# Kernel tuning notes

Measured on AMD Instinct MI355X. Metric: run time of the kernel, lower is better.

The kernel has to match this reference:

```python
import jax, jax.numpy as jnp
import numpy as np

N_SERIES = 1024
N_TIME = 600
INPUT_SIZE = 168
OUTPUT_SIZE = 24
N_S = 4
SEAS = 24  # single seasonality period


def setup_inputs() -> dict:
    key = jax.random.key(0)
    k1, k2, k3 = jax.random.split(key, 3)
    # strictly positive series (Holt-Winters multiplicative form divides and logs)
    y = jax.random.uniform(k1, (N_SERIES, N_TIME), jnp.float32) + 0.5
    s_matrix = jax.random.normal(k2, (N_SERIES, N_S), jnp.float32)
    embeds = jax.random.uniform(k3, (N_SERIES, 1 + 1 + SEAS), jnp.float32)
    idxs = jnp.arange(N_SERIES, dtype=jnp.int32)
    return {"y": y, "s_matrix": s_matrix, "embeds": embeds, "idxs": idxs}


def _compute_levels_seasons(y, embeds_rows):
    # embeds_rows: (N, 26) = [lev_sms_logit, seas_sms_logit, 24 log init seasons]
    lev_sms = jax.nn.sigmoid(embeds_rows[:, 0])           # (N,)
    seas_sms = jax.nn.sigmoid(embeds_rows[:, 1])          # (N,)
    init_seas = jnp.exp(embeds_rows[:, 2:2 + SEAS])       # (N, P)

    level0 = y[:, 0] / init_seas[:, 0]                    # (N,)
    # buffer holds seasonalities1[t .. t+P-1]; before step t=1 that is
    # [init[1], ..., init[P-1], init[0]]
    buf0 = jnp.roll(init_seas, -1, axis=1)                # (N, P)

    def step(carry, y_t):
        lev_prev, buf = carry
        s_t = buf[:, 0]
        newlev = lev_sms * (y_t / s_t) + (1.0 - lev_sms) * lev_prev
        news = seas_sms * (y_t / newlev) + (1.0 - seas_sms) * s_t
        buf = jnp.concatenate([buf[:, 1:], news[:, None]], axis=1)
        return (newlev, buf), (newlev, news)

    (_, _), (levs, seas_new) = jax.lax.scan(step, (level0, buf0), y[:, 1:].T)
    levels = jnp.concatenate([level0[:, None], levs.T], axis=1)          # (N, T)
    # seasonalities1 indices 0..P are [init[0..P-1], init[0]], then one new per step
    seas_head = jnp.concatenate([init_seas, init_seas[:, :1]], axis=1)   # (N, P+1)
    seasonalities1 = jnp.concatenate([seas_head, seas_new.T], axis=1)    # (N, T+P)
    return levels, seasonalities1


def reference(y, s_matrix, embeds, idxs):
    embeds_rows = embeds[idxs]                                 # (N, 26)
    levels, seasonalities1 = _compute_levels_seasons(y, embeds_rows)

    n_series, n_time = y.shape
    n_windows = n_time - INPUT_SIZE - OUTPUT_SIZE + 1          # 409
    w = jnp.arange(n_windows)
    idx_in = w[:, None] + jnp.arange(INPUT_SIZE)               # (W, I)
    idx_out = w[:, None] + INPUT_SIZE + jnp.arange(OUTPUT_SIZE)  # (W, O)

    y_in = y[:, idx_in]                                        # (N, W, I)
    lev_end = levels[:, w + INPUT_SIZE - 1]                    # (N, W)
    seas_in = seasonalities1[:, idx_in]                        # (N, W, I)
    y_in_norm = jnp.log(y_in / (lev_end[:, :, None] * seas_in))
    insample = jnp.transpose(y_in_norm, (1, 0, 2))             # (W, N, I)
    static = jnp.broadcast_to(s_matrix[None], (n_windows, n_series, s_matrix.shape[1]))
    windows_y_insample = jnp.concatenate([insample, static], axis=2)  # (W, N, I+n_s)

    # eval mode: outsample windows are raw (un-normalized) targets
    windows_y_outsample = jnp.transpose(y[:, idx_out], (1, 0, 2))     # (W, N, O)

    return (windows_y_insample, windows_y_outsample, levels, seasonalities1)
```

## Files before the change

### kernel.cpp

```cpp
#include <hip/hip_runtime.h>

#define N_SERIES 1024
#define N_TIME 600
#define INPUT_SIZE 168
#define OUTPUT_SIZE 24
#define N_S 4
#define SEAS 24
#define N_WINDOWS (N_TIME - INPUT_SIZE - OUTPUT_SIZE + 1)
#define SEAS_LEN (N_TIME + SEAS)

#define INS_ELEMS (N_WINDOWS * N_SERIES * (INPUT_SIZE + N_S))
#define OUTS_ELEMS (N_WINDOWS * N_SERIES * OUTPUT_SIZE)
#define LEV_ELEMS (N_SERIES * N_TIME)
#define SEAS_ELEMS (N_SERIES * SEAS_LEN)

#define NQ_OUTS (OUTS_ELEMS / 4)
#define NQ_INS43 (N_WINDOWS * N_SERIES * 43)
#define INS_SLICE (NQ_INS43 / 8)

#define SCAN_BLOCKS 16
#define SCAN_T 64
#define COPY_BLOCKS 2032
#define INS_BLOCKS 2048
#define WS_NEEDED (2u * LEV_ELEMS * sizeof(float))

typedef float f4 __attribute__((ext_vector_type(4)));

#define WAVE_FENCE()                                   \
    do {                                               \
        __builtin_amdgcn_wave_barrier();               \
        asm volatile("" ::: "memory");                 \
    } while (0)

__global__ __launch_bounds__(SCAN_T) void scan_copy_kernel(
    const float* __restrict__ y, const float* __restrict__ embeds,
    const int* __restrict__ idxs, float* __restrict__ levels,
    float* __restrict__ seas1, f4* __restrict__ out_outs)
{
    __shared__ float b_lev[SCAN_T][25];
    __shared__ float b_sea[SCAN_T][25];

    if (blockIdx.x < SCAN_BLOCKS) {
        const int lane = threadIdx.x;
        const int s0 = blockIdx.x * SCAN_T;
        const int s = s0 + lane;
        const int row = idxs[s];
        const float* e = embeds + row * (2 + SEAS);

        const float lev_sms = 1.0f / (1.0f + __expf(-e[0]));
        const float seas_sms = 1.0f / (1.0f + __expf(-e[1]));
        const float one_m_lev = 1.0f - lev_sms;
        const float one_m_seas = 1.0f - seas_sms;

        const float* yrow = y + s * N_TIME;
        const f4* yv4 = (const f4*)yrow;

        f4 cur[6], nxt[6];
#pragma unroll
        for (int i = 0; i < 6; ++i) cur[i] = yv4[i];

        float sb[SEAS];
#pragma unroll
        for (int j = 0; j < SEAS; ++j) {
            float v = __expf(e[2 + j]);
            sb[j] = v;
            b_sea[lane][j] = v;
        }
        WAVE_FENCE();
#pragma unroll
        for (int k4 = 0; k4 < 6; ++k4) {
            int q4 = lane + k4 * SCAN_T;
            int r = q4 / 6;
            int c4 = q4 - r * 6;
            int cc = c4 * 4;
            f4 v = {b_sea[r][cc], b_sea[r][cc + 1], b_sea[r][cc + 2],
                    b_sea[r][cc + 3]};
            *(f4*)(seas1 + (s0 + r) * SEAS_LEN + cc) = v;
        }
        seas1[s * SEAS_LEN + SEAS] = sb[0];
        float lev = __fdividef(cur[0].x, sb[0]);
        levels[s * N_TIME] = lev;
        WAVE_FENCE();

        {
#pragma unroll
            for (int i = 0; i < 6; ++i) nxt[i] = yv4[6 + i];
#pragma unroll
            for (int j = 0; j < 23; ++j) {
                const int t = j + 1;
                float yt = cur[t >> 2][t & 3];
                float st = sb[t];
                float q1 = __fdividef(yt, st);
                float newlev = lev_sms * q1 + one_m_lev * lev;
                float news =
                    seas_sms * __fdividef(yt, newlev) + one_m_seas * st;
                lev = newlev;
                sb[t] = news;
                b_lev[lane][j] = newlev;
                b_sea[lane][j] = news;
            }
            WAVE_FENCE();
#pragma unroll
            for (int k = 0; k < 24; ++k) {
                int i = lane + k * SCAN_T;
                int r = i / 24;
                int col = i - r * 24;
                if (col < 23) {
                    int sr = s0 + r;
                    levels[sr * N_TIME + 1 + col] = b_lev[r][col];
                    seas1[sr * SEAS_LEN + 25 + col] = b_sea[r][col];
                }
            }
            WAVE_FENCE();
#pragma unroll
            for (int i = 0; i < 6; ++i) cur[i] = nxt[i];
        }

#pragma unroll 1
        for (int c = 1; c < 25; ++c) {
            const int t0 = 24 * c;
            if (c < 24) {
                const f4* p = (const f4*)(yrow + 24 * (c + 1));
#pragma unroll
                for (int i = 0; i < 6; ++i) nxt[i] = p[i];
            }
#pragma unroll
            for (int j = 0; j < 24; ++j) {
                float yt = cur[j >> 2][j & 3];
                float st = sb[j];
                float q1 = __fdividef(yt, st);
                float newlev = lev_sms * q1 + one_m_lev * lev;
                float news =
                    seas_sms * __fdividef(yt, newlev) + one_m_seas * st;
                lev = newlev;
                sb[j] = news;
                b_lev[lane][j] = newlev;
                b_sea[lane][j] = news;
            }
            WAVE_FENCE();
#pragma unroll
            for (int k4 = 0; k4 < 6; ++k4) {
                int q4 = lane + k4 * SCAN_T;
                int r = q4 / 6;
                int c4 = q4 - r * 6;
                int sr = s0 + r;
                int cc = c4 * 4;
                f4 vl = {b_lev[r][cc], b_lev[r][cc + 1], b_lev[r][cc + 2],
                         b_lev[r][cc + 3]};
                *(f4*)(levels + sr * N_TIME + t0 + cc) = vl;
                f4 vs = {b_sea[r][cc], b_sea[r][cc + 1], b_sea[r][cc + 2],
                         b_sea[r][cc + 3]};
                *(f4*)(seas1 + sr * SEAS_LEN + SEAS + t0 + cc) = vs;
            }
            WAVE_FENCE();
#pragma unroll
            for (int i = 0; i < 6; ++i) cur[i] = nxt[i];
        }
    } else {
        int idx = (blockIdx.x - SCAN_BLOCKS) * SCAN_T + threadIdx.x;
        const int stride = (gridDim.x - SCAN_BLOCKS) * SCAN_T;
        for (; idx < NQ_OUTS; idx += stride) {
            int rowq = idx / 6;
            int j4 = idx - rowq * 6;
            int w = rowq >> 10;
            int s = rowq & 1023;
            const float* yp = y + s * N_TIME + w + INPUT_SIZE + j4 * 4;
            f4 v = {yp[0], yp[1], yp[2], yp[3]};
            out_outs[idx] = v;
        }
    }
}

__global__ __launch_bounds__(256) void logpass_kernel(
    const float* __restrict__ y, const float* __restrict__ levels,
    const float* __restrict__ seas1, float* __restrict__ tbl,
    float* __restrict__ llv)
{
    int i = blockIdx.x * 256 + threadIdx.x;
    int sr = i / 150;
    int c = i - sr * 150;
    f4 a = *((const f4*)(y + sr * N_TIME) + c);
    f4 se = *((const f4*)(seas1 + sr * SEAS_LEN) + c);
    f4 l = *((const f4*)(levels + sr * N_TIME) + c);
    f4 ta, tl;
    ta.x = __logf(__fdividef(a.x, se.x));
    ta.y = __logf(__fdividef(a.y, se.y));
    ta.z = __logf(__fdividef(a.z, se.z));
    ta.w = __logf(__fdividef(a.w, se.w));
    tl.x = __logf(l.x);
    tl.y = __logf(l.y);
    tl.z = __logf(l.z);
    tl.w = __logf(l.w);
    ((f4*)tbl)[i] = ta;
    ((f4*)llv)[i] = tl;
}

__global__ __launch_bounds__(256) void ins_kernel(
    const float* __restrict__ tbl, const float* __restrict__ llv,
    const float* __restrict__ s_matrix, f4* __restrict__ out_ins)
{
    const f4* sm4 = (const f4*)s_matrix;
    const int xcd = blockIdx.x & 7;
    const int lb = blockIdx.x >> 3;
    const int qend = (xcd + 1) * INS_SLICE;
    const int stride = (INS_BLOCKS / 8) * 256;
    for (int q = xcd * INS_SLICE + lb * 256 + (int)threadIdx.x; q < qend;
         q += stride) {
        int rowq = q / 43;
        int e4 = q - rowq * 43;
        int w = rowq >> 10;
        int s = rowq & 1023;
        f4 v;
        if (e4 == 42) {
            v = sm4[s];
        } else {
            int t = w + e4 * 4;
            const float* tp = tbl + s * N_TIME + t;
            float lv = llv[s * N_TIME + w + INPUT_SIZE - 1];
            v.x = tp[0] - lv;
            v.y = tp[1] - lv;
            v.z = tp[2] - lv;
            v.w = tp[3] - lv;
        }
        out_ins[q] = v;
    }
}

__global__ __launch_bounds__(256) void ins_kernel_fb(
    const float* __restrict__ y, const float* __restrict__ levels,
    const float* __restrict__ seas1, const float* __restrict__ s_matrix,
    f4* __restrict__ out_ins)
{
    const f4* sm4 = (const f4*)s_matrix;
    const int xcd = blockIdx.x & 7;
    const int lb = blockIdx.x >> 3;
    const int qend = (xcd + 1) * INS_SLICE;
    const int stride = (INS_BLOCKS / 8) * 256;
    for (int q = xcd * INS_SLICE + lb * 256 + (int)threadIdx.x; q < qend;
         q += stride) {
        int rowq = q / 43;
        int e4 = q - rowq * 43;
        int w = rowq >> 10;
        int s = rowq & 1023;
        f4 v;
        if (e4 == 42) {
            v = sm4[s];
        } else {
            int t = w + e4 * 4;
            float lev = levels[s * N_TIME + w + INPUT_SIZE - 1];
            const float* yp = y + s * N_TIME + t;
            const float* sp = seas1 + s * SEAS_LEN + t;
            float vv[4];
#pragma unroll
            for (int j = 0; j < 4; ++j)
                vv[j] = __logf(__fdividef(yp[j], lev * sp[j]));
            v.x = vv[0]; v.y = vv[1]; v.z = vv[2]; v.w = vv[3];
        }
        out_ins[q] = v;
    }
}

extern "C" void kernel_launch(void* const* d_in, const int* in_sizes, int n_in,
                              void* d_out, int out_size, void* d_ws, size_t ws_size,
                              hipStream_t stream) {
    const float* y      = (const float*)d_in[0];
    const float* sm     = (const float*)d_in[1];
    const float* embeds = (const float*)d_in[2];
    const int*   idxs   = (const int*)d_in[3];

    float* out      = (float*)d_out;
    float* out_ins  = out;
    float* out_outs = out + INS_ELEMS;
    float* out_lev  = out + INS_ELEMS + OUTS_ELEMS;
    float* out_seas = out_lev + LEV_ELEMS;

    float* tbl = (float*)d_ws;
    float* llv = tbl + LEV_ELEMS;
    const int have_ws = (ws_size >= (size_t)WS_NEEDED) ? 1 : 0;

    scan_copy_kernel<<<SCAN_BLOCKS + COPY_BLOCKS, SCAN_T, 0, stream>>>(
        y, embeds, idxs, out_lev, out_seas, (f4*)out_outs);
    if (have_ws) {
        logpass_kernel<<<LEV_ELEMS / 4 / 256, 256, 0, stream>>>(
            y, out_lev, out_seas, tbl, llv);
        ins_kernel<<<INS_BLOCKS, 256, 0, stream>>>(tbl, llv, sm,
                                                   (f4*)out_ins);
    } else {
        ins_kernel_fb<<<INS_BLOCKS, 256, 0, stream>>>(y, out_lev, out_seas,
                                                      sm, (f4*)out_ins);
    }
}
```

Before: 111.3 us.

## Assign series pairs per block in insample kernel and use nontemporal stores

```diff
diff --git a/kernel.cpp b/kernel.cpp
--- a/kernel.cpp
+++ b/kernel.cpp
@@ -15,14 +15,16 @@
 #define SEAS_ELEMS (N_SERIES * SEAS_LEN)
 
 #define NQ_OUTS (OUTS_ELEMS / 4)
-#define NQ_INS43 (N_WINDOWS * N_SERIES * 43)
-#define INS_SLICE (NQ_INS43 / 8)
 
 #define SCAN_BLOCKS 16
 #define SCAN_T 64
 #define COPY_BLOCKS 2032
-#define INS_BLOCKS 2048
 #define WS_NEEDED (2u * LEV_ELEMS * sizeof(float))
+
+#define INS2_BLOCKS 512
+#define SGRP 2
+#define TASKS_PER_W (SGRP * 43)
+#define TASKS_PER_G (N_WINDOWS * TASKS_PER_W)
 
 typedef float f4 __attribute__((ext_vector_type(4)));
 
@@ -166,7 +168,7 @@
             int s = rowq & 1023;
             const float* yp = y + s * N_TIME + w + INPUT_SIZE + j4 * 4;
             f4 v = {yp[0], yp[1], yp[2], yp[3]};
-            out_outs[idx] = v;
+            __builtin_nontemporal_store(v, &out_outs[idx]);
         }
     }
 }
@@ -195,25 +197,23 @@
     ((f4*)llv)[i] = tl;
 }
 
-__global__ __launch_bounds__(256) void ins_kernel(
+__global__ __launch_bounds__(256) void ins2_kernel(
     const float* __restrict__ tbl, const float* __restrict__ llv,
-    const float* __restrict__ s_matrix, f4* __restrict__ out_ins)
+    const float* __restrict__ y, const float* __restrict__ levels,
+    const float* __restrict__ seas1, const float* __restrict__ s_matrix,
+    f4* __restrict__ out_ins, int have_ws)
 {
-    const f4* sm4 = (const f4*)s_matrix;
-    const int xcd = blockIdx.x & 7;
-    const int lb = blockIdx.x >> 3;
-    const int qend = (xcd + 1) * INS_SLICE;
-    const int stride = (INS_BLOCKS / 8) * 256;
-    for (int q = xcd * INS_SLICE + lb * 256 + (int)threadIdx.x; q < qend;
-         q += stride) {
-        int rowq = q / 43;
-        int e4 = q - rowq * 43;
-        int w = rowq >> 10;
-        int s = rowq & 1023;
+    const int s0 = blockIdx.x * SGRP;
+    for (int ql = threadIdx.x; ql < TASKS_PER_G; ql += 256) {
+        int w = ql / TASKS_PER_W;
+        int slot = ql - w * TASKS_PER_W;
+        int sl = slot / 43;
+        int e4 = slot - sl * 43;
+        int s = s0 + sl;
         f4 v;
         if (e4 == 42) {
-            v = sm4[s];
-        } else {
+            v = *(const f4*)(s_matrix + s * N_S);
+        } else if (have_ws) {
             int t = w + e4 * 4;
             const float* tp = tbl + s * N_TIME + t;
             float lv = llv[s * N_TIME + w + INPUT_SIZE - 1];
@@ -221,42 +221,17 @@
             v.y = tp[1] - lv;
             v.z = tp[2] - lv;
             v.w = tp[3] - lv;
-        }
-        out_ins[q] = v;
-    }
-}
-
-__global__ __launch_bounds__(256) void ins_kernel_fb(
-    const float* __restrict__ y, const float* __restrict__ levels,
-    const float* __restrict__ seas1, const float* __restrict__ s_matrix,
-    f4* __restrict__ out_ins)
-{
-    const f4* sm4 = (const f4*)s_matrix;
-    const int xcd = blockIdx.x & 7;
-    const int lb = blockIdx.x >> 3;
-    const int qend = (xcd + 1) * INS_SLICE;
-    const int stride = (INS_BLOCKS / 8) * 256;
-    for (int q = xcd * INS_SLICE + lb * 256 + (int)threadIdx.x; q < qend;
-         q += stride) {
-        int rowq = q / 43;
-        int e4 = q - rowq * 43;
-        int w = rowq >> 10;
-        int s = rowq & 1023;
-        f4 v;
-        if (e4 == 42) {
-            v = sm4[s];
         } else {
             int t = w + e4 * 4;
             float lev = levels[s * N_TIME + w + INPUT_SIZE - 1];
             const float* yp = y + s * N_TIME + t;
             const float* sp = seas1 + s * SEAS_LEN + t;
-            float vv[4];
-#pragma unroll
-            for (int j = 0; j < 4; ++j)
-                vv[j] = __logf(__fdividef(yp[j], lev * sp[j]));
-            v.x = vv[0]; v.y = vv[1]; v.z = vv[2]; v.w = vv[3];
-        }
-        out_ins[q] = v;
+            v.x = __logf(__fdividef(yp[0], lev * sp[0]));
+            v.y = __logf(__fdividef(yp[1], lev * sp[1]));
+            v.z = __logf(__fdividef(yp[2], lev * sp[2]));
+            v.w = __logf(__fdividef(yp[3], lev * sp[3]));
+        }
+        __builtin_nontemporal_store(v, &out_ins[w * 44032 + s * 43 + e4]);
     }
 }
 
@@ -283,10 +258,7 @@
     if (have_ws) {
         logpass_kernel<<<LEV_ELEMS / 4 / 256, 256, 0, stream>>>(
             y, out_lev, out_seas, tbl, llv);
-        ins_kernel<<<INS_BLOCKS, 256, 0, stream>>>(tbl, llv, sm,
-                                                   (f4*)out_ins);
-    } else {
-        ins_kernel_fb<<<INS_BLOCKS, 256, 0, stream>>>(y, out_lev, out_seas,
-                                                      sm, (f4*)out_ins);
     }
-}
+    ins2_kernel<<<INS2_BLOCKS, 256, 0, stream>>>(
+        tbl, llv, y, out_lev, out_seas, sm, (f4*)out_ins, have_ws);
+}
```

Result: slower. 127.4 us (+14.5%).
